# Kernel optimization log

Hardware: AMD Instinct MI355X
Metric: run time of the kernel (lower is better)

## Reference

```python
import jax, jax.numpy as jnp
import numpy as np

EPS = 1e-8  # torch F.cosine_similarity norm clamp


def setup_inputs() -> dict:
    key = jax.random.key(0)
    k1, k2, k3, k4, k5 = jax.random.split(key, 5)
    C, S, H = 20000, 32, 256
    Cs = S // 2  # compressed_seq_len = int(S * 0.5)
    B = 64
    return {
        "query": jax.random.normal(k1, (B, H), dtype=jnp.float32),
        "episodes": jax.random.normal(k2, (C, S, H), dtype=jnp.float32),
        "compressed_episodes": jax.random.normal(k3, (C, Cs, H), dtype=jnp.float32),
        "episode_embeddings": jax.random.normal(k4, (C, H), dtype=jnp.float32),
        "is_compressed": jax.random.randint(k5, (C,), 0, 2) > 0,
        "k": 8,
    }


def reference(query, episodes, compressed_episodes, episode_embeddings, is_compressed, k):
    # Cosine similarity with torch-style eps clamping of each norm.
    qn = query / jnp.maximum(jnp.linalg.norm(query, axis=-1, keepdims=True), EPS)
    en = episode_embeddings / jnp.maximum(
        jnp.linalg.norm(episode_embeddings, axis=-1, keepdims=True), EPS
    )
    sims = qn @ en.T  # [B, C]

    top_scores, top_idx = jax.lax.top_k(sims, k)  # [B, k]

    B = query.shape[0]
    S, H = episodes.shape[1], episodes.shape[2]
    Cs = compressed_episodes.shape[1]

    full = episodes[top_idx]                 # [B, k, S, H] gather
    comp = compressed_episodes[top_idx]      # [B, k, Cs, H] gather
    pad = jnp.zeros((B, k, S - Cs, H), dtype=comp.dtype)
    padded = jnp.concatenate([comp, pad], axis=2)  # [B, k, S, H]

    mask = is_compressed[top_idx][:, :, None, None]  # [B, k, 1, 1]
    retrieved = jnp.where(mask, padded, full)        # [B, k, S, H]
    return retrieved, top_scores
```

## Files before the change

kernel.cpp:

```cpp
#include <hip/hip_runtime.h>
#include <math.h>

#define HDIM 256
#define H4   64
#define EPSN 1e-8f
#define CT   80
#define KC   8
#define NCH  8

typedef unsigned long long u64;
typedef unsigned int       u32;

__device__ __forceinline__ u64 make_key(float v, int idx) {
    u32 u = __float_as_uint(v);
    u ^= (u & 0x80000000u) ? 0xFFFFFFFFu : 0x80000000u;
    return ((u64)u << 32) | (u32)(~idx);
}
__device__ __forceinline__ float key_val(u64 k) {
    u32 u = (u32)(k >> 32);
    u ^= (u & 0x80000000u) ? 0x80000000u : 0xFFFFFFFFu;
    return __uint_as_float(u);
}
__device__ __forceinline__ int key_idx(u64 k) { return (int)(~(u32)k); }

__device__ __forceinline__ void insert8(u64* ls, u64 k) {
    if (k > ls[7]) {
        ls[7] = k;
        #pragma unroll
        for (int j = 7; j > 0; --j)
            if (ls[j] > ls[j-1]) { u64 tmp = ls[j]; ls[j] = ls[j-1]; ls[j-1] = tmp; }
    }
}

__global__ __launch_bounds__(256)
void sims_kernel(const float4* __restrict__ q4, const float4* __restrict__ emb4,
                 float* __restrict__ sims, int C, int B) {
    __shared__ float4 e_lds[2][CT][KC + 1];
    __shared__ float4 q_lds[2][64][KC + 1];

    const int t  = threadIdx.x;
    const int c0 = blockIdx.x * CT;
    const int tc = t & 15;
    const int tb = t >> 4;
    const float4 z = make_float4(0.f, 0.f, 0.f, 0.f);

    float4 pe0, pe1, pe2, pq0, pq1;

    #define LOAD_E(idx, ch, dst) do {                                        \
        int _r = (idx) >> 3, _cl = (idx) & 7; int _gc = c0 + _r;             \
        dst = (_gc < C) ? emb4[(size_t)_gc * H4 + (ch) * KC + _cl] : z;      \
    } while (0)
    #define LOAD_Q(idx, ch, dst) do {                                        \
        int _r = (idx) >> 3, _cl = (idx) & 7;                                \
        dst = (_r < B) ? q4[(size_t)_r * H4 + (ch) * KC + _cl] : z;          \
    } while (0)
    #define LOAD_CHUNK(ch) do {                                              \
        LOAD_E(t,       ch, pe0); LOAD_E(t + 256, ch, pe1);                  \
        if (t < 128) LOAD_E(t + 512, ch, pe2);                               \
        LOAD_Q(t,       ch, pq0); LOAD_Q(t + 256, ch, pq1);                  \
    } while (0)
    #define WRITE_CHUNK(pp) do {                                             \
        { int r = t >> 3,       cl = t & 7;       e_lds[pp][r][cl] = pe0; }  \
        { int r = (t+256) >> 3, cl = (t+256) & 7; e_lds[pp][r][cl] = pe1; }  \
        if (t < 128) { int r = (t+512) >> 3, cl = (t+512) & 7; e_lds[pp][r][cl] = pe2; } \
        { int r = t >> 3,       cl = t & 7;       q_lds[pp][r][cl] = pq0; }  \
        { int r = (t+256) >> 3, cl = (t+256) & 7; q_lds[pp][r][cl] = pq1; }  \
    } while (0)

    float acc[5][4], ee[5], qq[4];
    #pragma unroll
    for (int i = 0; i < 5; ++i) {
        ee[i] = 0.f;
        #pragma unroll
        for (int j = 0; j < 4; ++j) acc[i][j] = 0.f;
    }
    #pragma unroll
    for (int j = 0; j < 4; ++j) qq[j] = 0.f;

    LOAD_CHUNK(0);
    WRITE_CHUNK(0);
    __syncthreads();

    int p = 0;
    for (int ch = 0; ch < NCH; ++ch) {
        if (ch + 1 < NCH) LOAD_CHUNK(ch + 1);

        #pragma unroll
        for (int s = 0; s < KC; ++s) {
            float4 a[5], b[4];
            #pragma unroll
            for (int i = 0; i < 5; ++i) a[i] = e_lds[p][tc + 16 * i][s];
            #pragma unroll
            for (int j = 0; j < 4; ++j) b[j] = q_lds[p][tb + 16 * j][s];

            #pragma unroll
            for (int i = 0; i < 5; ++i)
                ee[i] = fmaf(a[i].x,a[i].x, fmaf(a[i].y,a[i].y,
                        fmaf(a[i].z,a[i].z, fmaf(a[i].w,a[i].w, ee[i]))));
            #pragma unroll
            for (int j = 0; j < 4; ++j)
                qq[j] = fmaf(b[j].x,b[j].x, fmaf(b[j].y,b[j].y,
                        fmaf(b[j].z,b[j].z, fmaf(b[j].w,b[j].w, qq[j]))));
            #pragma unroll
            for (int i = 0; i < 5; ++i)
                #pragma unroll
                for (int j = 0; j < 4; ++j)
                    acc[i][j] = fmaf(a[i].x,b[j].x, fmaf(a[i].y,b[j].y,
                                fmaf(a[i].z,b[j].z, fmaf(a[i].w,b[j].w, acc[i][j]))));
        }

        if (ch + 1 < NCH) {
            WRITE_CHUNK(p ^ 1);
            __syncthreads();
            p ^= 1;
        }
    }

    float einv[5], qinv[4];
    #pragma unroll
    for (int i = 0; i < 5; ++i) einv[i] = 1.f / fmaxf(sqrtf(ee[i]), EPSN);
    #pragma unroll
    for (int j = 0; j < 4; ++j) qinv[j] = 1.f / fmaxf(sqrtf(qq[j]), EPSN);

    #pragma unroll
    for (int j = 0; j < 4; ++j) {
        int b = tb + 16 * j;
        if (b < B) {
            #pragma unroll
            for (int i = 0; i < 5; ++i) {
                int c = c0 + tc + 16 * i;
                if (c < C) sims[(size_t)b * C + c] = acc[i][j] * qinv[j] * einv[i];
            }
        }
    }
    #undef WRITE_CHUNK
    #undef LOAD_CHUNK
    #undef LOAD_Q
    #undef LOAD_E
}

__global__ __launch_bounds__(256)
void topk_scan(const float* __restrict__ sims, const u32* __restrict__ mask4,
               u64* __restrict__ cand, int* __restrict__ flags, int C, int B) {
    const int t = threadIdx.x;

    if (blockIdx.x == (unsigned)(B * 4)) {
        __shared__ int red0[4], red1[4];
        int lo = 0, lg = 0;
        const int n4 = C >> 2;
        int i = t;
        for (; i + 768 < n4; i += 1024) {
            u32 v0 = mask4[i], v1 = mask4[i + 256], v2 = mask4[i + 512], v3 = mask4[i + 768];
            u32 o = v0 | v1 | v2 | v3;
            if (o & 0xFFFFFF00u) lo = 1;
            if (o & 0xFEFEFEFEu) lg = 1;
        }
        for (; i < n4; i += 256) {
            u32 v = mask4[i];
            if (v & 0xFFFFFF00u) lo = 1;
            if (v & 0xFEFEFEFEu) lg = 1;
        }
        const unsigned char* mb = (const unsigned char*)mask4;
        for (int j = (n4 << 2) + t; j < C; j += 256) {
            unsigned char v = mb[j];
            if (v > 1) lg = 1;
            if ((j & 3) != 0 && v != 0) lo = 1;
        }
        lo = __any(lo); lg = __any(lg);
        if ((t & 63) == 0) { red0[t >> 6] = lo; red1[t >> 6] = lg; }
        __syncthreads();
        if (t == 0) {
            flags[0] = red0[0] | red0[1] | red0[2] | red0[3];
            flags[1] = red1[0] | red1[1] | red1[2] | red1[3];
        }
        return;
    }

    __shared__ u64 sh[256 * 8];
    const int b    = blockIdx.x >> 2;
    const int seg  = blockIdx.x & 3;
    const int slen = (C + 3) >> 2;
    const int cbeg = seg * slen;
    const int cend = min(cbeg + slen, C);
    const float* row = sims + (size_t)b * C;

    u64 ls[8];
    #pragma unroll
    for (int j = 0; j < 8; ++j) ls[j] = 0ull;

    int c = cbeg + t;
    for (; c + 7 * 256 < cend; c += 8 * 256) {
        float v[8];
        #pragma unroll
        for (int u = 0; u < 8; ++u) v[u] = row[c + u * 256];
        #pragma unroll
        for (int u = 0; u < 8; ++u) insert8(ls, make_key(v[u], c + u * 256));
    }
    for (; c < cend; c += 256) insert8(ls, make_key(row[c], c));

    #pragma unroll
    for (int j = 0; j < 8; ++j) sh[t * 8 + j] = ls[j];
    __syncthreads();

    if (t < 64) {
        u64 m[8];
        #pragma unroll
        for (int j = 0; j < 8; ++j) m[j] = 0ull;
        for (int tt = 0; tt < 4; ++tt) {
            const u64* pp = &sh[(t * 4 + tt) * 8];
            #pragma unroll
            for (int j = 0; j < 8; ++j) {
                u64 k = pp[j];
                if (k <= m[7]) break;
                m[7] = k;
                #pragma unroll
                for (int q = 7; q > 0; --q)
                    if (m[q] > m[q-1]) { u64 tmp = m[q]; m[q] = m[q-1]; m[q-1] = tmp; }
            }
        }
        for (int r = 0; r < 8; ++r) {
            u64 best = m[0];
            #pragma unroll
            for (int off = 32; off; off >>= 1) {
                u64 o = __shfl_xor(best, off, 64);
                if (o > best) best = o;
            }
            if (m[0] == best) {
                #pragma unroll
                for (int q = 0; q < 7; ++q) m[q] = m[q+1];
                m[7] = 0ull;
            }
            if (t == 0) cand[((size_t)b * 4 + seg) * 8 + r] = best;
        }
    }
}

__global__ __launch_bounds__(256)
void gather_kernel(const float* __restrict__ episodes,
                   const float* __restrict__ compressed,
                   const void* __restrict__ is_comp,
                   const u64* __restrict__ cand,
                   const int* __restrict__ flags,
                   float* __restrict__ out,
                   float* __restrict__ scores_out,
                   int S, int Cs) {
    const int bj = blockIdx.x >> 1;
    const int h  = blockIdx.x & 1;
    const int b  = bj >> 3;
    const int j  = bj & 7;

    const u64* cb = cand + (size_t)b * 32;
    u64 ls[8];
    #pragma unroll
    for (int q = 0; q < 8; ++q) ls[q] = 0ull;
    #pragma unroll
    for (int i = 0; i < 32; ++i) insert8(ls, cb[i]);

    const u64 kj  = ls[j];
    const int idx = key_idx(kj);
    if (h == 0 && threadIdx.x == 0) scores_out[bj] = key_val(kj);

    const int f_off = flags[0], f_gt1 = flags[1];
    bool comp;
    if      (f_gt1) comp = ((const float*)is_comp)[idx] != 0.f;
    else if (f_off) comp = ((const unsigned char*)is_comp)[idx] != 0;
    else            comp = ((const int*)is_comp)[idx] != 0;

    const int n4   = S * H4;
    const int c4   = Cs * H4;
    const int half = n4 >> 1;
    const int v0   = h * half;

    const float4* full4 = (const float4*)episodes   + (size_t)idx * n4;
    const float4* cmp4  = (const float4*)compressed + (size_t)idx * c4;
    float4* out4 = (float4*)out + (size_t)bj * n4;
    const float4 z = make_float4(0.f, 0.f, 0.f, 0.f);

    if (comp) {
        #pragma unroll 4
        for (int v = v0 + threadIdx.x; v < v0 + half; v += 256)
            out4[v] = (v < c4) ? cmp4[v] : z;
    } else {
        #pragma unroll 4
        for (int v = v0 + threadIdx.x; v < v0 + half; v += 256)
            out4[v] = full4[v];
    }
}

extern "C" void kernel_launch(void* const* d_in, const int* in_sizes, int n_in,
                              void* d_out, int out_size, void* d_ws, size_t ws_size,
                              hipStream_t stream) {
    const float* query      = (const float*)d_in[0];
    const float* episodes   = (const float*)d_in[1];
    const float* compressed = (const float*)d_in[2];
    const float* emb        = (const float*)d_in[3];
    const void*  is_comp    = d_in[4];

    const int B  = in_sizes[0] / HDIM;
    const int C  = in_sizes[3] / HDIM;
    const int S  = in_sizes[1] / (C * HDIM);
    const int Cs = in_sizes[2] / (C * HDIM);
    const int K  = 8;

    float* out        = (float*)d_out;
    float* scores_out = out + (size_t)B * K * S * HDIM;

    float* sims    = (float*)d_ws;
    size_t simsOff = (((size_t)B * C * sizeof(float)) + 255) & ~(size_t)255;
    u64*   cand    = (u64*)((char*)d_ws + simsOff);
    int*   flags   = (int*)(cand + (size_t)B * 32);

    sims_kernel<<<(C + CT - 1) / CT, 256, 0, stream>>>(
        (const float4*)query, (const float4*)emb, sims, C, B);
    topk_scan<<<B * 4 + 1, 256, 0, stream>>>(sims, (const u32*)is_comp,
                                             cand, flags, C, B);
    gather_kernel<<<B * K * 2, 256, 0, stream>>>(episodes, compressed, is_comp,
                                                 cand, flags, out, scores_out,
                                                 S, Cs);
}
```

Before: 55.42 us.

## Fuse per-tile top-8 selection into sims kernel and merge candidates separately

The similarity kernel now stages its 64x80 score tile in shared memory, aliased with the staging buffers through a union. Each group of 20 columns then produces a local top-8 per query, so the full B x C similarity matrix is never written to global memory. A new merge kernel reduces the NT*32 candidates per query to the final top-8 and writes scores and indices. The gather kernel reads those precomputed indices and splits each episode copy across four blocks instead of two. The trade-off is more candidate traffic (64*250*32 u64 keys) and a serial insert loop in the epilogue of the sims kernel.

```diff
diff --git a/kernel.cpp b/kernel.cpp
--- a/kernel.cpp
+++ b/kernel.cpp
@@ -5,6 +5,7 @@
 #define H4   64
 #define EPSN 1e-8f
 #define CT   80
+#define GP   20
 #define KC   8
 #define NCH  8
 
@@ -33,10 +34,13 @@
 }
 
 __global__ __launch_bounds__(256)
-void sims_kernel(const float4* __restrict__ q4, const float4* __restrict__ emb4,
-                 float* __restrict__ sims, int C, int B) {
-    __shared__ float4 e_lds[2][CT][KC + 1];
-    __shared__ float4 q_lds[2][64][KC + 1];
+void sims_topk_kernel(const float4* __restrict__ q4,
+                      const float4* __restrict__ emb4,
+                      u64* __restrict__ cand, int C, int B, int NT) {
+    __shared__ union SMu {
+        struct St { float4 e[2][CT][KC + 1]; float4 q[2][64][KC + 1]; } st;
+        struct Ep { float sc[64][CT + 1]; } ep;
+    } sm;
 
     const int t  = threadIdx.x;
     const int c0 = blockIdx.x * CT;
@@ -60,11 +64,11 @@
         LOAD_Q(t,       ch, pq0); LOAD_Q(t + 256, ch, pq1);                  \
     } while (0)
     #define WRITE_CHUNK(pp) do {                                             \
-        { int r = t >> 3,       cl = t & 7;       e_lds[pp][r][cl] = pe0; }  \
-        { int r = (t+256) >> 3, cl = (t+256) & 7; e_lds[pp][r][cl] = pe1; }  \
-        if (t < 128) { int r = (t+512) >> 3, cl = (t+512) & 7; e_lds[pp][r][cl] = pe2; } \
-        { int r = t >> 3,       cl = t & 7;       q_lds[pp][r][cl] = pq0; }  \
-        { int r = (t+256) >> 3, cl = (t+256) & 7; q_lds[pp][r][cl] = pq1; }  \
+        { int r = t >> 3,       cl = t & 7;       sm.st.e[pp][r][cl] = pe0; }\
+        { int r = (t+256) >> 3, cl = (t+256) & 7; sm.st.e[pp][r][cl] = pe1; }\
+        if (t < 128) { int r = (t+512) >> 3, cl = (t+512) & 7; sm.st.e[pp][r][cl] = pe2; } \
+        { int r = t >> 3,       cl = t & 7;       sm.st.q[pp][r][cl] = pq0; }\
+        { int r = (t+256) >> 3, cl = (t+256) & 7; sm.st.q[pp][r][cl] = pq1; }\
     } while (0)
 
     float acc[5][4], ee[5], qq[4];
@@ -89,9 +93,9 @@
         for (int s = 0; s < KC; ++s) {
             float4 a[5], b[4];
             #pragma unroll
-            for (int i = 0; i < 5; ++i) a[i] = e_lds[p][tc + 16 * i][s];
-            #pragma unroll
-            for (int j = 0; j < 4; ++j) b[j] = q_lds[p][tb + 16 * j][s];
+            for (int i = 0; i < 5; ++i) a[i] = sm.st.e[p][tc + 16 * i][s];
+            #pragma unroll
+            for (int j = 0; j < 4; ++j) b[j] = sm.st.q[p][tb + 16 * j][s];
 
             #pragma unroll
             for (int i = 0; i < 5; ++i)
@@ -122,16 +126,33 @@
     #pragma unroll
     for (int j = 0; j < 4; ++j) qinv[j] = 1.f / fmaxf(sqrtf(qq[j]), EPSN);
 
+    __syncthreads();
     #pragma unroll
     for (int j = 0; j < 4; ++j) {
         int b = tb + 16 * j;
         if (b < B) {
             #pragma unroll
-            for (int i = 0; i < 5; ++i) {
-                int c = c0 + tc + 16 * i;
-                if (c < C) sims[(size_t)b * C + c] = acc[i][j] * qinv[j] * einv[i];
-            }
-        }
+            for (int i = 0; i < 5; ++i)
+                sm.ep.sc[b][tc + 16 * i] = acc[i][j] * qinv[j] * einv[i];
+        }
+    }
+    __syncthreads();
+
+    const int sb = t & 63;
+    const int g  = t >> 6;
+    if (sb < B) {
+        u64 ls[8];
+        #pragma unroll
+        for (int j = 0; j < 8; ++j) ls[j] = 0ull;
+        #pragma unroll
+        for (int i2 = 0; i2 < GP; ++i2) {
+            int cl = g * GP + i2;
+            int c  = c0 + cl;
+            if (c < C) insert8(ls, make_key(sm.ep.sc[sb][cl], c));
+        }
+        u64* dst = cand + (((size_t)sb * NT + blockIdx.x) * 4 + g) * 8;
+        #pragma unroll
+        for (int r = 0; r < 8; ++r) dst[r] = ls[r];
     }
     #undef WRITE_CHUNK
     #undef LOAD_CHUNK
@@ -140,11 +161,12 @@
 }
 
 __global__ __launch_bounds__(256)
-void topk_scan(const float* __restrict__ sims, const u32* __restrict__ mask4,
-               u64* __restrict__ cand, int* __restrict__ flags, int C, int B) {
+void merge_kernel(const u64* __restrict__ cand, const u32* __restrict__ mask4,
+                  float* __restrict__ scores_out, int* __restrict__ top_idx,
+                  int* __restrict__ flags, int C, int B, int NT) {
     const int t = threadIdx.x;
 
-    if (blockIdx.x == (unsigned)(B * 4)) {
+    if (blockIdx.x == (unsigned)B) {
         __shared__ int red0[4], red1[4];
         int lo = 0, lg = 0;
         const int n4 = C >> 2;
@@ -177,60 +199,60 @@
     }
 
     __shared__ u64 sh[256 * 8];
-    const int b    = blockIdx.x >> 2;
-    const int seg  = blockIdx.x & 3;
-    const int slen = (C + 3) >> 2;
-    const int cbeg = seg * slen;
-    const int cend = min(cbeg + slen, C);
-    const float* row = sims + (size_t)b * C;
+    const int b     = blockIdx.x;
+    const int total = NT * 32;
+    const u64* cb   = cand + (size_t)b * total;
 
     u64 ls[8];
     #pragma unroll
     for (int j = 0; j < 8; ++j) ls[j] = 0ull;
 
-    int c = cbeg + t;
-    for (; c + 7 * 256 < cend; c += 8 * 256) {
-        float v[8];
-        #pragma unroll
-        for (int u = 0; u < 8; ++u) v[u] = row[c + u * 256];
-        #pragma unroll
-        for (int u = 0; u < 8; ++u) insert8(ls, make_key(v[u], c + u * 256));
-    }
-    for (; c < cend; c += 256) insert8(ls, make_key(row[c], c));
+    int m = t;
+    for (; m + 7 * 256 < total; m += 8 * 256) {
+        u64 v[8];
+        #pragma unroll
+        for (int u = 0; u < 8; ++u) v[u] = cb[m + u * 256];
+        #pragma unroll
+        for (int u = 0; u < 8; ++u) insert8(ls, v[u]);
+    }
+    for (; m < total; m += 256) insert8(ls, cb[m]);
 
     #pragma unroll
     for (int j = 0; j < 8; ++j) sh[t * 8 + j] = ls[j];
     __syncthreads();
 
     if (t < 64) {
-        u64 m[8];
-        #pragma unroll
-        for (int j = 0; j < 8; ++j) m[j] = 0ull;
+        u64 mr[8];
+        #pragma unroll
+        for (int j = 0; j < 8; ++j) mr[j] = 0ull;
         for (int tt = 0; tt < 4; ++tt) {
             const u64* pp = &sh[(t * 4 + tt) * 8];
             #pragma unroll
             for (int j = 0; j < 8; ++j) {
                 u64 k = pp[j];
-                if (k <= m[7]) break;
-                m[7] = k;
+                if (k <= mr[7]) break;
+                mr[7] = k;
                 #pragma unroll
                 for (int q = 7; q > 0; --q)
-                    if (m[q] > m[q-1]) { u64 tmp = m[q]; m[q] = m[q-1]; m[q-1] = tmp; }
+                    if (mr[q] > mr[q-1]) { u64 tmp = mr[q]; mr[q] = mr[q-1]; mr[q-1] = tmp; }
             }
         }
         for (int r = 0; r < 8; ++r) {
-            u64 best = m[0];
+            u64 best = mr[0];
             #pragma unroll
             for (int off = 32; off; off >>= 1) {
                 u64 o = __shfl_xor(best, off, 64);
                 if (o > best) best = o;
             }
-            if (m[0] == best) {
+            if (mr[0] == best) {
                 #pragma unroll
-                for (int q = 0; q < 7; ++q) m[q] = m[q+1];
-                m[7] = 0ull;
+                for (int q = 0; q < 7; ++q) mr[q] = mr[q+1];
+                mr[7] = 0ull;
             }
-            if (t == 0) cand[((size_t)b * 4 + seg) * 8 + r] = best;
+            if (t == 0) {
+                scores_out[b * 8 + r] = key_val(best);
+                top_idx[b * 8 + r]    = key_idx(best);
+            }
         }
     }
 }
@@ -239,37 +261,24 @@
 void gather_kernel(const float* __restrict__ episodes,
                    const float* __restrict__ compressed,
                    const void* __restrict__ is_comp,
-                   const u64* __restrict__ cand,
+                   const int* __restrict__ top_idx,
                    const int* __restrict__ flags,
                    float* __restrict__ out,
-                   float* __restrict__ scores_out,
                    int S, int Cs) {
-    const int bj = blockIdx.x >> 1;
-    const int h  = blockIdx.x & 1;
-    const int b  = bj >> 3;
-    const int j  = bj & 7;
-
-    const u64* cb = cand + (size_t)b * 32;
-    u64 ls[8];
-    #pragma unroll
-    for (int q = 0; q < 8; ++q) ls[q] = 0ull;
-    #pragma unroll
-    for (int i = 0; i < 32; ++i) insert8(ls, cb[i]);
-
-    const u64 kj  = ls[j];
-    const int idx = key_idx(kj);
-    if (h == 0 && threadIdx.x == 0) scores_out[bj] = key_val(kj);
-
+    const int bj  = blockIdx.x >> 2;
+    const int qtr = blockIdx.x & 3;
+    const int idx = top_idx[bj];
     const int f_off = flags[0], f_gt1 = flags[1];
+
     bool comp;
     if      (f_gt1) comp = ((const float*)is_comp)[idx] != 0.f;
     else if (f_off) comp = ((const unsigned char*)is_comp)[idx] != 0;
     else            comp = ((const int*)is_comp)[idx] != 0;
 
-    const int n4   = S * H4;
-    const int c4   = Cs * H4;
-    const int half = n4 >> 1;
-    const int v0   = h * half;
+    const int n4    = S * H4;
+    const int c4    = Cs * H4;
+    const int qlen  = n4 >> 2;
+    const int v0    = qtr * qlen;
 
     const float4* full4 = (const float4*)episodes   + (size_t)idx * n4;
     const float4* cmp4  = (const float4*)compressed + (size_t)idx * c4;
@@ -277,12 +286,12 @@
     const float4 z = make_float4(0.f, 0.f, 0.f, 0.f);
 
     if (comp) {
-        #pragma unroll 4
-        for (int v = v0 + threadIdx.x; v < v0 + half; v += 256)
+        #pragma unroll 2
+        for (int v = v0 + threadIdx.x; v < v0 + qlen; v += 256)
             out4[v] = (v < c4) ? cmp4[v] : z;
     } else {
-        #pragma unroll 4
-        for (int v = v0 + threadIdx.x; v < v0 + half; v += 256)
+        #pragma unroll 2
+        for (int v = v0 + threadIdx.x; v < v0 + qlen; v += 256)
             out4[v] = full4[v];
     }
 }
@@ -301,20 +310,19 @@
     const int S  = in_sizes[1] / (C * HDIM);
     const int Cs = in_sizes[2] / (C * HDIM);
     const int K  = 8;
+    const int NT = (C + CT - 1) / CT;
 
     float* out        = (float*)d_out;
     float* scores_out = out + (size_t)B * K * S * HDIM;
 
-    float* sims    = (float*)d_ws;
-    size_t simsOff = (((size_t)B * C * sizeof(float)) + 255) & ~(size_t)255;
-    u64*   cand    = (u64*)((char*)d_ws + simsOff);
-    int*   flags   = (int*)(cand + (size_t)B * 32);
-
-    sims_kernel<<<(C + CT - 1) / CT, 256, 0, stream>>>(
-        (const float4*)query, (const float4*)emb, sims, C, B);
-    topk_scan<<<B * 4 + 1, 256, 0, stream>>>(sims, (const u32*)is_comp,
-                                             cand, flags, C, B);
-    gather_kernel<<<B * K * 2, 256, 0, stream>>>(episodes, compressed, is_comp,
-                                                 cand, flags, out, scores_out,
-                                                 S, Cs);
-}
+    u64*  cand    = (u64*)d_ws;
+    int*  top_idx = (int*)(cand + (size_t)B * NT * 32);
+    int*  flags   = top_idx + B * K;
+
+    sims_topk_kernel<<<NT, 256, 0, stream>>>(
+        (const float4*)query, (const float4*)emb, cand, C, B, NT);
+    merge_kernel<<<B + 1, 256, 0, stream>>>(cand, (const u32*)is_comp,
+                                            scores_out, top_idx, flags, C, B, NT);
+    gather_kernel<<<B * K * 4, 256, 0, stream>>>(episodes, compressed, is_comp,
+                                                 top_idx, flags, out, S, Cs);
+}
```

Measured after the change: 59.14 us. +6.7%, slower.
